# Performance work log

Measured on AMD Instinct MI355X. Metric: run time of the kernel, lower is better.

The kernel has to match this reference:

```python
import jax, jax.numpy as jnp
import numpy as np

T, H = 8192, 2048


def setup_inputs() -> dict:
    key = jax.random.key(0)
    k1, k2, k3 = jax.random.split(key, 3)
    x_sequence = jax.random.normal(k1, (T, H), dtype=jnp.float32)
    lamda = jax.random.normal(k2, (H,), dtype=jnp.float32) * 0.2
    B = jax.random.normal(k3, (H, H), dtype=jnp.float32) / np.sqrt(H).astype(np.float32)
    return {"x_sequence": x_sequence, "lamda": lamda, "B": B}


def reference(x_sequence, lamda, B):
    # Batched input projection: u_t = B @ x_t for all t -> one GEMM. [T, H]
    u = x_sequence @ B.T
    # Linear diagonal recurrence h_t = lamda * h_{t-1} + u_t with h_0 = 0,
    # solved with a log-depth associative scan over (a, b) pairs where
    # combine((a1,b1),(a2,b2)) = (a2*a1, a2*b1 + b2).
    a = jnp.broadcast_to(lamda, u.shape)  # [T, H]

    def combine(c1, c2):
        a1, b1 = c1
        a2, b2 = c2
        return (a2 * a1, a2 * b1 + b2)

    _, h = jax.lax.associative_scan(combine, (a, u))
    return h  # [T, H] stacked hidden states
```

## Files before the change

### kernel.cpp

```cpp
#include <hip/hip_runtime.h>
#include <hip/hip_bf16.h>


#define TDIM 8192
#define HDIM 2048
#define BM 256
#define BN 256
#define KT 64
#define NIT (HDIM / KT)
#define SLOT 16384
#define LCH 64
#define GCH (TDIM / LCH)

typedef float f32x4 __attribute__((ext_vector_type(4)));
typedef short s16x4 __attribute__((ext_vector_type(4)));
typedef short s16x8 __attribute__((ext_vector_type(8)));

static __device__ __forceinline__ short f2bf(float f) {
  __bf16 b = (__bf16)f;
  return __builtin_bit_cast(short, b);
}

__global__ __launch_bounds__(512, 2) void gemm_fused2(
    const float* __restrict__ X, const float* __restrict__ Bm,
    const float* __restrict__ lam,
    float* __restrict__ U, float* __restrict__ e) {
  extern __shared__ __align__(16) short smem[];
  short* As = smem;
  short* Bs = smem + 2 * SLOT;

  const int wg  = blockIdx.x;
  const int swz = (wg & 7) * 32 + (wg >> 3);
  const int tm = swz >> 3;
  const int tn = swz & 7;
  const int row0 = tm * BM, col0 = tn * BN;

  const int tid  = threadIdx.x;
  const int lane = tid & 63;
  const int wid  = tid >> 6;
  const int wr = (wid >> 2) * 128;
  const int wc = (wid & 3) * 64;

  const int g4 = lane >> 4;
  int offA[8], offB[4];
#pragma unroll
  for (int m = 0; m < 8; ++m) {
    const int r = wr + m * 16 + (lane & 15);
    offA[m] = r * 64 + ((g4 ^ (r & 3)) << 3) + (((r >> 2) & 1) << 5);
  }
#pragma unroll
  for (int n = 0; n < 4; ++n) {
    const int r = wc + n * 16 + (lane & 15);
    offB[n] = r * 64 + ((g4 ^ (r & 3)) << 3) + (((r >> 2) & 1) << 5);
  }

  const int lrow   = tid >> 4;
  const int lcol16 = (tid & 15) * 4;
  const float* gA = X  + (size_t)(row0 + lrow) * HDIM + lcol16;
  const float* gB = Bm + (size_t)(col0 + lrow) * HDIM + lcol16;

  int offW[8];
#pragma unroll
  for (int c = 0; c < 8; ++c) {
    const int wrow = lrow + c * 32;
    offW[c] = wrow * 64 + ((((tid & 15) >> 1) ^ (wrow & 7)) << 3) + (tid & 1) * 4;
  }

#define ISSUE(dst, gp, t_) do {                                               \
    _Pragma("unroll") for (int c = 0; c < 8; ++c)                             \
      dst[c] = *(const f32x4*)((gp) + (size_t)c * 32 * HDIM + (t_) * KT);     \
  } while (0)

#define CVTWR(arr, base, sl) do {                                             \
    _Pragma("unroll") for (int c = 0; c < 8; ++c) {                           \
      s16x4 v;                                                                \
      v[0] = f2bf(arr[c][0]); v[1] = f2bf(arr[c][1]);                         \
      v[2] = f2bf(arr[c][2]); v[3] = f2bf(arr[c][3]);                         \
      *(s16x4*)&base[(sl) * SLOT + offW[c]] = v;                              \
    }                                                                         \
  } while (0)

#define PHASE(sl, khx) do {                                                   \
    s16x8 af[8], bfv[4];                                                      \
    _Pragma("unroll") for (int m = 0; m < 8; ++m)                             \
      af[m] = *(const s16x8*)&As[(sl) * SLOT + (offA[m] ^ (khx))];            \
    _Pragma("unroll") for (int n = 0; n < 4; ++n)                             \
      bfv[n] = *(const s16x8*)&Bs[(sl) * SLOT + (offB[n] ^ (khx))];           \
    __builtin_amdgcn_s_setprio(1);                                            \
    _Pragma("unroll") for (int m = 0; m < 8; ++m)                             \
      _Pragma("unroll") for (int n = 0; n < 4; ++n)                           \
        acc[m][n] = __builtin_amdgcn_mfma_f32_16x16x32_bf16(                  \
            af[m], bfv[n], acc[m][n], 0, 0, 0);                               \
    __builtin_amdgcn_s_setprio(0);                                            \
  } while (0)

  f32x4 acc[8][4] = {};
  f32x4 ra[8], rb[8];

  ISSUE(ra, gA, 0);
  ISSUE(rb, gB, 0);
  CVTWR(ra, As, 0);
  CVTWR(rb, Bs, 0);
  __syncthreads();

  for (int j = 0; j < NIT - 1; ++j) {
    const int cur = j & 1;
    ISSUE(ra, gA, j + 1);
    PHASE(cur, 0);
    CVTWR(ra, As, cur ^ 1);
    ISSUE(rb, gB, j + 1);
    PHASE(cur, 32);
    CVTWR(rb, Bs, cur ^ 1);
    __syncthreads();
  }
  {
    const int cur = (NIT - 1) & 1;
    PHASE(cur, 0);
    PHASE(cur, 32);
  }

  const int crow = row0 + wr + (g4 << 2);
  const int ccol = col0 + wc + (lane & 15);
#pragma unroll
  for (int m = 0; m < 8; ++m)
#pragma unroll
    for (int n = 0; n < 4; ++n)
#pragma unroll
      for (int j = 0; j < 4; ++j)
        U[(size_t)(crow + m * 16 + j) * HDIM + ccol + n * 16] = acc[m][n][j];

#pragma unroll
  for (int n = 0; n < 4; ++n) {
    const int c = ccol + n * 16;
    const float l  = lam[c];
    const float l2 = l * l;
    const float l4 = l2 * l2;
    const float l8 = l4 * l4;
    const float l16 = l8 * l8;
    float lg = 1.f;
    if (g4 < 3) lg = l4;
    if (g4 < 2) lg *= l4;
    if (g4 < 1) lg *= l4;
#pragma unroll
    for (int half = 0; half < 2; ++half) {
      float S = 0.f;
#pragma unroll
      for (int mq = 0; mq < 4; ++mq) {
        const f32x4 a = acc[half * 4 + mq][n];
        const float T = ((a[0] * l + a[1]) * l + a[2]) * l + a[3];
        S = S * l16 + T;
      }
      S *= lg;
      S += __shfl_xor(S, 16, 64);
      S += __shfl_xor(S, 32, 64);
      if (g4 == 0) {
        const int j = tm * 4 + (wr >> 6) + half;
        e[(size_t)j * HDIM + c] = S;
      }
    }
  }

#undef ISSUE
#undef CVTWR
#undef PHASE
}

__global__ __launch_bounds__(256, 2) void gemm_f32_fb(
    const float* __restrict__ X, const float* __restrict__ Bm,
    float* __restrict__ U) {
#define LDK 40
#define FBM 128
#define FBK 32
#define FNT (HDIM / FBK)
  __shared__ __align__(16) short As[2][FBM * LDK];
  __shared__ __align__(16) short Bs[2][FBM * LDK];
  const int wg  = blockIdx.x;
  const int cpx = (TDIM / FBM) * (HDIM / FBM) / 8;
  const int swz = (wg & 7) * cpx + (wg >> 3);
  const int tm = swz >> 4;
  const int tn = swz & 15;
  const int row0 = tm * FBM, col0 = tn * FBM;
  const int tid  = threadIdx.x;
  const int lane = tid & 63;
  const int wid  = tid >> 6;
  const int wr = (wid >> 1) * 64;
  const int wc = (wid & 1) * 64;
  const int srow = tid >> 2;
  const int sk   = (tid & 3) << 3;
  const float* gA  = X  + (size_t)(row0 + srow) * HDIM + sk;
  const float* gA2 = gA + 64 * HDIM;
  const float* gB  = Bm + (size_t)(col0 + srow) * HDIM + sk;
  const float* gB2 = gB + 64 * HDIM;
  f32x4 a00, a01, a10, a11, b00, b01, b10, b11;
#define LOADREG(kt) do {                                                      \
    const float* p;                                                           \
    p = gA  + (kt) * FBK; a00 = *(const f32x4*)p; a01 = *(const f32x4*)(p+4); \
    p = gA2 + (kt) * FBK; a10 = *(const f32x4*)p; a11 = *(const f32x4*)(p+4); \
    p = gB  + (kt) * FBK; b00 = *(const f32x4*)p; b01 = *(const f32x4*)(p+4); \
    p = gB2 + (kt) * FBK; b10 = *(const f32x4*)p; b11 = *(const f32x4*)(p+4); \
  } while (0)
#define CVT8(v, lo, hi) do {                                                  \
    v[0] = f2bf(lo[0]); v[1] = f2bf(lo[1]); v[2] = f2bf(lo[2]);               \
    v[3] = f2bf(lo[3]); v[4] = f2bf(hi[0]); v[5] = f2bf(hi[1]);               \
    v[6] = f2bf(hi[2]); v[7] = f2bf(hi[3]);                                   \
  } while (0)
#define DSWRITE(buf) do {                                                     \
    s16x8 v;                                                                  \
    CVT8(v, a00, a01); *(s16x8*)&As[buf][srow * LDK + sk] = v;                \
    CVT8(v, a10, a11); *(s16x8*)&As[buf][(srow + 64) * LDK + sk] = v;         \
    CVT8(v, b00, b01); *(s16x8*)&Bs[buf][srow * LDK + sk] = v;                \
    CVT8(v, b10, b11); *(s16x8*)&Bs[buf][(srow + 64) * LDK + sk] = v;         \
  } while (0)
  f32x4 acc[4][4] = {};
#define COMPUTE(buf) do {                                                     \
    const int r16_ = lane & 15;                                               \
    const int ks_  = (lane >> 4) * 8;                                         \
    s16x8 af[4], bfr[4];                                                      \
    _Pragma("unroll") for (int m = 0; m < 4; ++m)                             \
      af[m] = *(const s16x8*)&As[buf][(wr + m * 16 + r16_) * LDK + ks_];      \
    _Pragma("unroll") for (int n = 0; n < 4; ++n)                             \
      bfr[n] = *(const s16x8*)&Bs[buf][(wc + n * 16 + r16_) * LDK + ks_];     \
    _Pragma("unroll") for (int m = 0; m < 4; ++m)                             \
      _Pragma("unroll") for (int n = 0; n < 4; ++n)                           \
        acc[m][n] = __builtin_amdgcn_mfma_f32_16x16x32_bf16(                  \
            af[m], bfr[n], acc[m][n], 0, 0, 0);                               \
  } while (0)
  LOADREG(0);
  DSWRITE(0);
  __syncthreads();
#pragma unroll 2
  for (int kt = 0; kt < FNT; ++kt) {
    const int cur = kt & 1;
    if (kt + 1 < FNT) LOADREG(kt + 1);
    COMPUTE(cur);
    if (kt + 1 < FNT) DSWRITE(cur ^ 1);
    __syncthreads();
  }
  const int crow = wr + ((lane >> 4) << 2);
  const int ccol = wc + (lane & 15);
#pragma unroll
  for (int m = 0; m < 4; ++m)
#pragma unroll
    for (int n = 0; n < 4; ++n)
#pragma unroll
      for (int j = 0; j < 4; ++j)
        U[(size_t)(row0 + crow + m * 16 + j) * HDIM + (col0 + ccol + n * 16)] =
            acc[m][n][j];
#undef LOADREG
#undef CVT8
#undef DSWRITE
#undef COMPUTE
#undef LDK
#undef FBM
#undef FBK
#undef FNT
}

__global__ void scan_pass1(const float* __restrict__ U,
                           const float* __restrict__ lam,
                           float* __restrict__ e) {
  const int c = (blockIdx.y * 256 + threadIdx.x) * 4;
  const int j = blockIdx.x;
  const f32x4 l4 = *(const f32x4*)&lam[c];
  f32x4 h = {0.f, 0.f, 0.f, 0.f};
  const float* up = U + (size_t)j * LCH * HDIM + c;
#pragma unroll 4
  for (int t = 0; t < LCH; ++t) {
    f32x4 u4 = *(const f32x4*)up;
    h = l4 * h + u4;
    up += HDIM;
  }
  *(f32x4*)&e[(size_t)j * HDIM + c] = h;
}

__global__ void scan_carry(float* __restrict__ e, const float* __restrict__ lam) {
  const int c = (blockIdx.x * 256 + threadIdx.x) * 4;
  const f32x4 l4 = *(const f32x4*)&lam[c];
  f32x4 p = l4;
#pragma unroll
  for (int i = 0; i < 6; ++i) p = p * p;
  f32x4 E = {0.f, 0.f, 0.f, 0.f};
  for (int j = 0; j < GCH; ++j) {
    f32x4 ej = *(const f32x4*)&e[(size_t)j * HDIM + c];
    *(f32x4*)&e[(size_t)j * HDIM + c] = E;
    E = p * E + ej;
  }
}

__global__ void scan_pass3(float* __restrict__ U, const float* __restrict__ lam,
                           const float* __restrict__ carry) {
  const int c = (blockIdx.y * 256 + threadIdx.x) * 4;
  const int j = blockIdx.x;
  const f32x4 l4 = *(const f32x4*)&lam[c];
  f32x4 h = *(const f32x4*)&carry[(size_t)j * HDIM + c];
  float* up = U + (size_t)j * LCH * HDIM + c;
#pragma unroll 4
  for (int t = 0; t < LCH; ++t) {
    f32x4 u4 = *(const f32x4*)up;
    h = l4 * h + u4;
    *(f32x4*)up = h;
    up += HDIM;
  }
}

extern "C" void kernel_launch(void* const* d_in, const int* in_sizes, int n_in,
                              void* d_out, int out_size, void* d_ws, size_t ws_size,
                              hipStream_t stream) {
  const float* X   = (const float*)d_in[0];
  const float* lam = (const float*)d_in[1];
  const float* Bm  = (const float*)d_in[2];
  float* U = (float*)d_out;
  float* e = (float*)d_ws;

  if (ws_size >= (size_t)GCH * HDIM * 4) {
    hipFuncSetAttribute((const void*)gemm_fused2,
                        hipFuncAttributeMaxDynamicSharedMemorySize, 131072);
    gemm_fused2<<<dim3((TDIM / BM) * (HDIM / BN)), dim3(512), 131072, stream>>>(
        X, Bm, lam, U, e);
    scan_carry<<<dim3(HDIM / 1024), dim3(256), 0, stream>>>(e, lam);
    scan_pass3<<<dim3(GCH, HDIM / 1024), dim3(256), 0, stream>>>(U, lam, e);
  } else {
    gemm_f32_fb<<<dim3((TDIM / 128) * (HDIM / 128)), dim3(256), 0, stream>>>(
        X, Bm, U);
    scan_pass1<<<dim3(GCH, HDIM / 1024), dim3(256), 0, stream>>>(U, lam, e);
    scan_carry<<<dim3(HDIM / 1024), dim3(256), 0, stream>>>(e, lam);
    scan_pass3<<<dim3(GCH, HDIM / 1024), dim3(256), 0, stream>>>(U, lam, e);
  }
}
```

Before: 109.6 us.

## Pre-convert B to bf16, load it with global_load_lds, and fuse carry into pass3

Adds a pre-pass that converts B to bf16 in the workspace, so the GEMM streams B straight into LDS with global_load_lds instead of loading fp32 and converting in registers. The GEMM moves to a 128x256 tile with 256 threads, K-step 32 and static LDS, which raises the grid to 512 blocks. The serial scan_carry kernel is removed: each pass3 block recomputes its own carry prefix from the chunk sums, trading redundant work for one fewer launch and less serialisation. It needs a larger workspace, and if the workspace is too small the code falls back to the old path.

```diff
diff --git a/kernel.cpp b/kernel.cpp
--- a/kernel.cpp
+++ b/kernel.cpp
@@ -4,13 +4,18 @@
 
 #define TDIM 8192
 #define HDIM 2048
-#define BM 256
+#define BM 128
 #define BN 256
-#define KT 64
-#define NIT (HDIM / KT)
-#define SLOT 16384
+#define BK 32
+#define NIT (HDIM / BK)
+#define ASLOT 4096
+#define BSLOT 8192
 #define LCH 64
 #define GCH (TDIM / LCH)
+
+#define BBF_BYTES (HDIM * HDIM * 2)
+#define E_BYTES   (GCH * HDIM * 4)
+#define WS_NEED   ((size_t)BBF_BYTES + E_BYTES)
 
 typedef float f32x4 __attribute__((ext_vector_type(4)));
 typedef short s16x4 __attribute__((ext_vector_type(4)));
@@ -21,16 +26,37 @@
   return __builtin_bit_cast(short, b);
 }
 
-__global__ __launch_bounds__(512, 2) void gemm_fused2(
-    const float* __restrict__ X, const float* __restrict__ Bm,
+#define GL(gp, lp)                                                            \
+  __builtin_amdgcn_global_load_lds(                                           \
+      (const __attribute__((address_space(1))) void*)(gp),                    \
+      (__attribute__((address_space(3))) void*)(lp), 16, 0, 0)
+
+__global__ void cvt_B(const float* __restrict__ src, short* __restrict__ dst) {
+  const int base = blockIdx.x * 1024;
+  const int t = threadIdx.x;
+  f32x4 v0 = *(const f32x4*)(src + (size_t)(base +   0 + t) * 4);
+  f32x4 v1 = *(const f32x4*)(src + (size_t)(base + 256 + t) * 4);
+  f32x4 v2 = *(const f32x4*)(src + (size_t)(base + 512 + t) * 4);
+  f32x4 v3 = *(const f32x4*)(src + (size_t)(base + 768 + t) * 4);
+#define STORE1(v_, off_) do {                                                 \
+    s16x4 o;                                                                  \
+    o[0] = f2bf(v_[0]); o[1] = f2bf(v_[1]);                                   \
+    o[2] = f2bf(v_[2]); o[3] = f2bf(v_[3]);                                   \
+    *(s16x4*)(dst + (size_t)(base + (off_) + t) * 4) = o;                     \
+  } while (0)
+  STORE1(v0, 0); STORE1(v1, 256); STORE1(v2, 512); STORE1(v3, 768);
+#undef STORE1
+}
+
+__global__ __launch_bounds__(256, 2) void gemm_hyb2(
+    const float* __restrict__ X, const short* __restrict__ Bb,
     const float* __restrict__ lam,
     float* __restrict__ U, float* __restrict__ e) {
-  extern __shared__ __align__(16) short smem[];
-  short* As = smem;
-  short* Bs = smem + 2 * SLOT;
+  __shared__ __align__(16) short As[2][ASLOT];
+  __shared__ __align__(16) short Bs[2][BSLOT];
 
   const int wg  = blockIdx.x;
-  const int swz = (wg & 7) * 32 + (wg >> 3);
+  const int swz = (wg & 7) * 64 + (wg >> 3);
   const int tm = swz >> 3;
   const int tn = swz & 7;
   const int row0 = tm * BM, col0 = tn * BN;
@@ -38,99 +64,95 @@
   const int tid  = threadIdx.x;
   const int lane = tid & 63;
   const int wid  = tid >> 6;
-  const int wr = (wid >> 2) * 128;
-  const int wc = (wid & 3) * 64;
-
-  const int g4 = lane >> 4;
-  int offA[8], offB[4];
-#pragma unroll
-  for (int m = 0; m < 8; ++m) {
-    const int r = wr + m * 16 + (lane & 15);
-    offA[m] = r * 64 + ((g4 ^ (r & 3)) << 3) + (((r >> 2) & 1) << 5);
-  }
-#pragma unroll
-  for (int n = 0; n < 4; ++n) {
-    const int r = wc + n * 16 + (lane & 15);
-    offB[n] = r * 64 + ((g4 ^ (r & 3)) << 3) + (((r >> 2) & 1) << 5);
-  }
-
-  const int lrow   = tid >> 4;
-  const int lcol16 = (tid & 15) * 4;
-  const float* gA = X  + (size_t)(row0 + lrow) * HDIM + lcol16;
-  const float* gB = Bm + (size_t)(col0 + lrow) * HDIM + lcol16;
-
-  int offW[8];
-#pragma unroll
-  for (int c = 0; c < 8; ++c) {
-    const int wrow = lrow + c * 32;
-    offW[c] = wrow * 64 + ((((tid & 15) >> 1) ^ (wrow & 7)) << 3) + (tid & 1) * 4;
-  }
-
-#define ISSUE(dst, gp, t_) do {                                               \
-    _Pragma("unroll") for (int c = 0; c < 8; ++c)                             \
-      dst[c] = *(const f32x4*)((gp) + (size_t)c * 32 * HDIM + (t_) * KT);     \
-  } while (0)
-
-#define CVTWR(arr, base, sl) do {                                             \
-    _Pragma("unroll") for (int c = 0; c < 8; ++c) {                           \
+  const int wr = (wid >> 1) * 64;
+  const int wc = (wid & 1) * 128;
+  const int r16 = lane & 15;
+  const int g4  = lane >> 4;
+
+  int offA[4], offB[8];
+#pragma unroll
+  for (int m = 0; m < 4; ++m) {
+    const int r = wr + m * 16 + r16;
+    offA[m] = r * 32 + ((g4 ^ ((r >> 1) & 3)) << 3);
+  }
+#pragma unroll
+  for (int n = 0; n < 8; ++n) {
+    const int r = wc + n * 16 + r16;
+    offB[n] = r * 32 + ((g4 ^ ((r >> 1) & 3)) << 3);
+  }
+
+  const float* gA = X + (size_t)(row0 + (tid >> 3)) * HDIM + (tid & 7) * 4;
+  const int offWbase = (((((tid & 7) >> 1) ^ ((tid >> 4) & 3)) << 3) + (tid & 1) * 4)
+                       + (tid >> 3) * 32;
+
+  const int sgB = (tid & 3) ^ ((tid >> 3) & 3);
+  const short* gB = Bb + (size_t)(col0 + (tid >> 2)) * HDIM + sgB * 8;
+
+#define ISSUE_A(dst, t_) do {                                                 \
+    _Pragma("unroll") for (int c = 0; c < 4; ++c)                             \
+      dst[c] = *(const f32x4*)(gA + (size_t)c * 32 * HDIM + (t_) * BK);       \
+  } while (0)
+
+#define CVTWR_A(arr, sl) do {                                                 \
+    _Pragma("unroll") for (int c = 0; c < 4; ++c) {                           \
       s16x4 v;                                                                \
       v[0] = f2bf(arr[c][0]); v[1] = f2bf(arr[c][1]);                         \
       v[2] = f2bf(arr[c][2]); v[3] = f2bf(arr[c][3]);                         \
-      *(s16x4*)&base[(sl) * SLOT + offW[c]] = v;                              \
+      *(s16x4*)&As[sl][offWbase + c * 32 * 32] = v;                           \
     }                                                                         \
   } while (0)
 
-#define PHASE(sl, khx) do {                                                   \
-    s16x8 af[8], bfv[4];                                                      \
-    _Pragma("unroll") for (int m = 0; m < 8; ++m)                             \
-      af[m] = *(const s16x8*)&As[(sl) * SLOT + (offA[m] ^ (khx))];            \
-    _Pragma("unroll") for (int n = 0; n < 4; ++n)                             \
-      bfv[n] = *(const s16x8*)&Bs[(sl) * SLOT + (offB[n] ^ (khx))];           \
+#define GLOADB(sl, t_) do {                                                   \
+    _Pragma("unroll") for (int c = 0; c < 4; ++c)                             \
+      GL(gB + (size_t)c * 64 * HDIM + (t_) * BK,                              \
+         &Bs[sl][(c * 256 + tid) * 8]);                                       \
+  } while (0)
+
+#define PHASE(sl) do {                                                        \
+    s16x8 af[4], bfv[8];                                                      \
+    _Pragma("unroll") for (int m = 0; m < 4; ++m)                             \
+      af[m] = *(const s16x8*)&As[sl][offA[m]];                                \
+    _Pragma("unroll") for (int n = 0; n < 8; ++n)                             \
+      bfv[n] = *(const s16x8*)&Bs[sl][offB[n]];                               \
     __builtin_amdgcn_s_setprio(1);                                            \
-    _Pragma("unroll") for (int m = 0; m < 8; ++m)                             \
-      _Pragma("unroll") for (int n = 0; n < 4; ++n)                           \
+    _Pragma("unroll") for (int m = 0; m < 4; ++m)                             \
+      _Pragma("unroll") for (int n = 0; n < 8; ++n)                           \
         acc[m][n] = __builtin_amdgcn_mfma_f32_16x16x32_bf16(                  \
             af[m], bfv[n], acc[m][n], 0, 0, 0);                               \
     __builtin_amdgcn_s_setprio(0);                                            \
   } while (0)
 
-  f32x4 acc[8][4] = {};
-  f32x4 ra[8], rb[8];
-
-  ISSUE(ra, gA, 0);
-  ISSUE(rb, gB, 0);
-  CVTWR(ra, As, 0);
-  CVTWR(rb, Bs, 0);
+  f32x4 acc[4][8] = {};
+  f32x4 ra[4];
+
+  ISSUE_A(ra, 0);
+  GLOADB(0, 0);
+  CVTWR_A(ra, 0);
   __syncthreads();
 
+#pragma unroll 2
   for (int j = 0; j < NIT - 1; ++j) {
     const int cur = j & 1;
-    ISSUE(ra, gA, j + 1);
-    PHASE(cur, 0);
-    CVTWR(ra, As, cur ^ 1);
-    ISSUE(rb, gB, j + 1);
-    PHASE(cur, 32);
-    CVTWR(rb, Bs, cur ^ 1);
+    ISSUE_A(ra, j + 1);
+    GLOADB(cur ^ 1, j + 1);
+    PHASE(cur);
+    CVTWR_A(ra, cur ^ 1);
     __syncthreads();
   }
-  {
-    const int cur = (NIT - 1) & 1;
-    PHASE(cur, 0);
-    PHASE(cur, 32);
-  }
+  PHASE((NIT - 1) & 1);
 
   const int crow = row0 + wr + (g4 << 2);
-  const int ccol = col0 + wc + (lane & 15);
-#pragma unroll
-  for (int m = 0; m < 8; ++m)
-#pragma unroll
-    for (int n = 0; n < 4; ++n)
+  const int ccol = col0 + wc + r16;
+#pragma unroll
+  for (int m = 0; m < 4; ++m)
+#pragma unroll
+    for (int n = 0; n < 8; ++n)
 #pragma unroll
       for (int j = 0; j < 4; ++j)
         U[(size_t)(crow + m * 16 + j) * HDIM + ccol + n * 16] = acc[m][n][j];
 
 #pragma unroll
-  for (int n = 0; n < 4; ++n) {
+  for (int n = 0; n < 8; ++n) {
     const int c = ccol + n * 16;
     const float l  = lam[c];
     const float l2 = l * l;
@@ -141,28 +163,50 @@
     if (g4 < 3) lg = l4;
     if (g4 < 2) lg *= l4;
     if (g4 < 1) lg *= l4;
-#pragma unroll
-    for (int half = 0; half < 2; ++half) {
-      float S = 0.f;
-#pragma unroll
-      for (int mq = 0; mq < 4; ++mq) {
-        const f32x4 a = acc[half * 4 + mq][n];
-        const float T = ((a[0] * l + a[1]) * l + a[2]) * l + a[3];
-        S = S * l16 + T;
-      }
-      S *= lg;
-      S += __shfl_xor(S, 16, 64);
-      S += __shfl_xor(S, 32, 64);
-      if (g4 == 0) {
-        const int j = tm * 4 + (wr >> 6) + half;
-        e[(size_t)j * HDIM + c] = S;
-      }
+    float S = 0.f;
+#pragma unroll
+    for (int m = 0; m < 4; ++m) {
+      const f32x4 a = acc[m][n];
+      const float T = ((a[0] * l + a[1]) * l + a[2]) * l + a[3];
+      S = S * l16 + T;
     }
-  }
-
-#undef ISSUE
-#undef CVTWR
+    S *= lg;
+    S += __shfl_xor(S, 16, 64);
+    S += __shfl_xor(S, 32, 64);
+    if (g4 == 0) {
+      const int j = tm * 2 + (wid >> 1);
+      e[(size_t)j * HDIM + c] = S;
+    }
+  }
+
+#undef ISSUE_A
+#undef CVTWR_A
+#undef GLOADB
 #undef PHASE
+}
+
+__global__ void pass3f(float* __restrict__ U, const float* __restrict__ lam,
+                       const float* __restrict__ e) {
+  const int c = (blockIdx.y * 256 + threadIdx.x) * 4;
+  const int j = blockIdx.x;
+  const f32x4 l4 = *(const f32x4*)&lam[c];
+  f32x4 p = l4;
+#pragma unroll
+  for (int i = 0; i < 6; ++i) p = p * p;
+  f32x4 E = {0.f, 0.f, 0.f, 0.f};
+  for (int jp = 0; jp < j; ++jp) {
+    f32x4 ej = *(const f32x4*)&e[(size_t)jp * HDIM + c];
+    E = p * E + ej;
+  }
+  float* up = U + (size_t)j * LCH * HDIM + c;
+  f32x4 h = E;
+#pragma unroll 4
+  for (int t = 0; t < LCH; ++t) {
+    f32x4 u4 = *(const f32x4*)up;
+    h = l4 * h + u4;
+    *(f32x4*)up = h;
+    up += HDIM;
+  }
 }
 
 __global__ __launch_bounds__(256, 2) void gemm_f32_fb(
@@ -273,36 +317,6 @@
   *(f32x4*)&e[(size_t)j * HDIM + c] = h;
 }
 
-__global__ void scan_carry(float* __restrict__ e, const float* __restrict__ lam) {
-  const int c = (blockIdx.x * 256 + threadIdx.x) * 4;
-  const f32x4 l4 = *(const f32x4*)&lam[c];
-  f32x4 p = l4;
-#pragma unroll
-  for (int i = 0; i < 6; ++i) p = p * p;
-  f32x4 E = {0.f, 0.f, 0.f, 0.f};
-  for (int j = 0; j < GCH; ++j) {
-    f32x4 ej = *(const f32x4*)&e[(size_t)j * HDIM + c];
-    *(f32x4*)&e[(size_t)j * HDIM + c] = E;
-    E = p * E + ej;
-  }
-}
-
-__global__ void scan_pass3(float* __restrict__ U, const float* __restrict__ lam,
-                           const float* __restrict__ carry) {
-  const int c = (blockIdx.y * 256 + threadIdx.x) * 4;
-  const int j = blockIdx.x;
-  const f32x4 l4 = *(const f32x4*)&lam[c];
-  f32x4 h = *(const f32x4*)&carry[(size_t)j * HDIM + c];
-  float* up = U + (size_t)j * LCH * HDIM + c;
-#pragma unroll 4
-  for (int t = 0; t < LCH; ++t) {
-    f32x4 u4 = *(const f32x4*)up;
-    h = l4 * h + u4;
-    *(f32x4*)up = h;
-    up += HDIM;
-  }
-}
-
 extern "C" void kernel_launch(void* const* d_in, const int* in_sizes, int n_in,
                               void* d_out, int out_size, void* d_ws, size_t ws_size,
                               hipStream_t stream) {
@@ -310,20 +324,20 @@
   const float* lam = (const float*)d_in[1];
   const float* Bm  = (const float*)d_in[2];
   float* U = (float*)d_out;
-  float* e = (float*)d_ws;
-
-  if (ws_size >= (size_t)GCH * HDIM * 4) {
-    hipFuncSetAttribute((const void*)gemm_fused2,
-                        hipFuncAttributeMaxDynamicSharedMemorySize, 131072);
-    gemm_fused2<<<dim3((TDIM / BM) * (HDIM / BN)), dim3(512), 131072, stream>>>(
-        X, Bm, lam, U, e);
-    scan_carry<<<dim3(HDIM / 1024), dim3(256), 0, stream>>>(e, lam);
-    scan_pass3<<<dim3(GCH, HDIM / 1024), dim3(256), 0, stream>>>(U, lam, e);
+
+  if (ws_size >= WS_NEED) {
+    short* Bb = (short*)d_ws;
+    float* e  = (float*)((char*)d_ws + BBF_BYTES);
+
+    cvt_B<<<dim3(HDIM * HDIM / 4096), dim3(256), 0, stream>>>(Bm, Bb);
+    gemm_hyb2<<<dim3((TDIM / BM) * (HDIM / BN)), dim3(256), 0, stream>>>(
+        X, Bb, lam, U, e);
+    pass3f<<<dim3(GCH, HDIM / 1024), dim3(256), 0, stream>>>(U, lam, e);
   } else {
+    float* e = (float*)d_ws;
     gemm_f32_fb<<<dim3((TDIM / 128) * (HDIM / 128)), dim3(256), 0, stream>>>(
         X, Bm, U);
     scan_pass1<<<dim3(GCH, HDIM / 1024), dim3(256), 0, stream>>>(U, lam, e);
-    scan_carry<<<dim3(HDIM / 1024), dim3(256), 0, stream>>>(e, lam);
-    scan_pass3<<<dim3(GCH, HDIM / 1024), dim3(256), 0, stream>>>(U, lam, e);
-  }
-}
+    pass3f<<<dim3(GCH, HDIM / 1024), dim3(256), 0, stream>>>(U, lam, e);
+  }
+}
```

Result: slower. 127.0 us (+15.9%).
